# Kernel optimization log

Measured on AMD Instinct MI355X. Metric: run time of the kernel, lower is better.

## Reference

```python
import jax, jax.numpy as jnp
import numpy as np
import math

HEAD_DIM = 128
LAMBDA_INIT = 0.8
GN_EPS = 1e-05
NEG = -1e9


def ghostmax(scores):
    # softmax with an extra implicit zero logit (softmax-plus-one)
    m = jnp.maximum(jnp.max(scores, axis=-1, keepdims=True), 0.0)
    e = jnp.exp(scores - m)
    return e / (jnp.sum(e, axis=-1, keepdims=True) + jnp.exp(-m))


def setup_inputs() -> dict:
    key = jax.random.key(0)
    ks = jax.random.split(key, 8)
    B, H2, H, S, D = 2, 16, 8, 2048, HEAD_DIM
    return {
        "q": jax.random.normal(ks[0], (B, H2, S, D), dtype=jnp.float32),
        "k": jax.random.normal(ks[1], (B, H2, S, D), dtype=jnp.float32),
        "v": jax.random.normal(ks[2], (B, H, S, D), dtype=jnp.float32),
        "lambda_q1": 0.1 * jax.random.normal(ks[3], (D,), dtype=jnp.float32),
        "lambda_k1": 0.1 * jax.random.normal(ks[4], (D,), dtype=jnp.float32),
        "lambda_q2": 0.1 * jax.random.normal(ks[5], (D,), dtype=jnp.float32),
        "lambda_k2": 0.1 * jax.random.normal(ks[6], (D,), dtype=jnp.float32),
        "gn_weight": jnp.ones((H * D,), dtype=jnp.float32),
        "gn_bias": jnp.zeros((H * D,), dtype=jnp.float32),
    }


def reference(q, k, v, lambda_q1, lambda_k1, lambda_q2, lambda_k2, gn_weight, gn_bias):
    B, H2, S, D = q.shape
    H = H2 // 2
    scaling = 1.0 / math.sqrt(D)
    # [B, 2H, S, S] attention scores
    scores = jnp.einsum("bhsd,bhtd->bhst", q, k) * scaling
    causal_mask = jnp.triu(jnp.full((S, S), NEG, dtype=scores.dtype), k=1)
    scores = scores + causal_mask[None, None]
    w = ghostmax(scores)
    w = w.reshape(B, H, 2, S, S)
    lam = (
        jnp.exp(jnp.sum(lambda_q1 * lambda_k1))
        - jnp.exp(jnp.sum(lambda_q2 * lambda_k2))
        + LAMBDA_INIT
    )
    w = w[:, :, 0] - lam * w[:, :, 1]  # [B, H, S, S]
    out = jnp.einsum("bhst,bhtd->bhsd", w, v)  # [B, H, S, D]
    # torch .reshape(B, -1, S): raw row-major reinterpretation
    out = out.reshape(B, H * D, S)
    # GroupNorm: num_groups=H over channels H*D, normalized over (group channels, seq)
    g = out.reshape(B, H, D * S)
    mean = jnp.mean(g, axis=-1, keepdims=True)
    var = jnp.var(g, axis=-1, keepdims=True)
    g = (g - mean) * jax.lax.rsqrt(var + GN_EPS)
    out = g.reshape(B, H * D, S) * gn_weight[None, :, None] + gn_bias[None, :, None]
    return out * (1.0 - LAMBDA_INIT)
```

## Files before the change

### kernel.cpp

```cpp
#include <hip/hip_runtime.h>
#include <hip/hip_bf16.h>
#include <cstddef>
#include <cstdint>


typedef __bf16 bf16x8 __attribute__((ext_vector_type(8)));
typedef __bf16 bf16x4 __attribute__((ext_vector_type(4)));
typedef float f32x4 __attribute__((ext_vector_type(4)));

constexpr int SEQ = 2048;
constexpr int DH  = 128;
constexpr int NH  = 8;
constexpr int NH2 = 16;
constexpr float SCALE  = 0.088388347648318447f;
constexpr float QSCALE = 0.127517430f;

template <bool B> struct BoolK { static constexpr bool value = B; };

constexpr size_t QK_ELEMS = (size_t)2 * NH2 * SEQ * DH;
constexpr size_t V_ELEMS  = (size_t)2 * NH  * SEQ * DH;
constexpr size_t OFF_KB   = 4096;
constexpr size_t OFF_VT   = OFF_KB + QK_ELEMS * 2;
constexpr size_t WS_NEED  = OFF_VT + V_ELEMS * 2;

__device__ __forceinline__ void load_lds16(const void* g, void* l) {
  __builtin_amdgcn_global_load_lds(
      (const __attribute__((address_space(1))) uint32_t*)g,
      (__attribute__((address_space(3))) uint32_t*)l, 16, 0, 0);
}

__device__ __forceinline__ bf16x8 cvt8(float4 a, float4 b) {
  bf16x8 r;
  r[0] = (__bf16)a.x; r[1] = (__bf16)a.y; r[2] = (__bf16)a.z; r[3] = (__bf16)a.w;
  r[4] = (__bf16)b.x; r[5] = (__bf16)b.y; r[6] = (__bf16)b.z; r[7] = (__bf16)b.w;
  return r;
}

__global__ __launch_bounds__(256) void prep_kernel(
    const float* __restrict__ k, const float* __restrict__ v,
    __bf16* __restrict__ Kb, __bf16* __restrict__ Vtb,
    float* __restrict__ stats)
{
  __shared__ float tile[32][33];
  const int id = blockIdx.x;
  if (id == 0 && threadIdx.x < 64) stats[threadIdx.x] = 0.f;
  if (id < 4096) {
    const size_t i = ((size_t)id * 256 + threadIdx.x) * 8;
    float4 a = *(const float4*)(k + i);
    float4 b = *(const float4*)(k + i + 4);
    *(bf16x8*)(Kb + i) = cvt8(a, b);
  } else {
    const int vid = id - 4096;
    const int tt = vid & 63, dt = (vid >> 6) & 3, bh = vid >> 8;
    const int tr = threadIdx.x >> 3, tc = (threadIdx.x & 7) * 4;
    const float* src = v + ((size_t)bh * SEQ + tt * 32) * DH + dt * 32;
    float4 f = *(const float4*)(src + (size_t)tr * DH + tc);
    tile[tr][tc + 0] = f.x; tile[tr][tc + 1] = f.y;
    tile[tr][tc + 2] = f.z; tile[tr][tc + 3] = f.w;
    __syncthreads();
    __bf16* dst = Vtb + ((size_t)bh * DH + dt * 32 + tr) * SEQ + tt * 32 + tc;
    bf16x4 o;
    o[0] = (__bf16)tile[tc + 0][tr];
    o[1] = (__bf16)tile[tc + 1][tr];
    o[2] = (__bf16)tile[tc + 2][tr];
    o[3] = (__bf16)tile[tc + 3][tr];
    *(bf16x4*)dst = o;
  }
}

__global__ __launch_bounds__(256, 2) void attn3_kernel(
    const float* __restrict__ Qf, const __bf16* __restrict__ Kb,
    const __bf16* __restrict__ Vtb,
    const float* __restrict__ lq1, const float* __restrict__ lk1,
    const float* __restrict__ lq2, const float* __restrict__ lk2,
    float* __restrict__ Obuf, float* __restrict__ stats)
{
  __shared__ __align__(16) __bf16 ldsK[2][2][32][128];
  __shared__ __align__(16) __bf16 ldsVt[2][128][32];
  __shared__ __align__(16) __bf16 ldsP[4][32][36];
  __shared__ float ldsLa[64];

  const int bid = (int)blockIdx.x;
  int qt, bh;
  if (bid < 256) { qt = 31 - (bid >> 4); bh = bid & 15; }
  else           { qt = (bid - 256) >> 4; bh = bid & 15; }
  const int b = bh >> 3, h = bh & 7;
  const int tid = threadIdx.x;
  const int wv = tid >> 6;
  const int g  = wv >> 1;
  const int w2 = wv & 1;
  const int lane = tid & 63;
  const int l15 = lane & 15, quad = lane >> 4;

  float a1 = lq1[lane]*lk1[lane] + lq1[lane+64]*lk1[lane+64];
  float a2 = lq2[lane]*lk2[lane] + lq2[lane+64]*lk2[lane+64];
  #pragma unroll
  for (int off = 1; off < 64; off <<= 1) {
    a1 += __shfl_xor(a1, off);
    a2 += __shfl_xor(a2, off);
  }
  const float lam = __expf(a1) - __expf(a2) + 0.8f;

  const size_t headQK = (size_t)(b*NH2 + 2*h + g) * SEQ * DH;
  const float*  Qh  = Qf + headQK;
  const __bf16* Kh  = Kb + headQK;
  const __bf16* Vth = Vtb + (size_t)(b*NH + h) * DH * SEQ;

  size_t goffK[4];
  #pragma unroll
  for (int i = 0; i < 4; ++i) {
    const int c  = i*128 + w2*64 + lane;
    const int R  = c >> 4, cs = c & 15;
    goffK[i] = (size_t)R * DH + ((cs ^ (R & 15)) * 8);
  }
  size_t goffV[2];
  #pragma unroll
  for (int i = 0; i < 2; ++i) {
    const int c  = i*256 + tid;
    const int d  = c >> 2, cs = c & 3;
    goffV[i] = (size_t)d * SEQ + ((cs ^ (d & 3)) * 8);
  }

  __bf16* ldsKg = &ldsK[g][0][0][0];
  __bf16* ldsVb = &ldsVt[0][0][0];

  const int qb = qt * 64;
  const int nsteps = 2*qt + 2;
  const int rbase = qb + w2*32;

  bf16x8 qf[2][4];
  #pragma unroll
  for (int mi = 0; mi < 2; ++mi) {
    const float* src = Qh + (size_t)(rbase + mi*16 + l15)*DH + quad*8;
    #pragma unroll
    for (int kd = 0; kd < 4; ++kd) {
      float4 f0 = *(const float4*)(src + kd*32);
      float4 f1 = *(const float4*)(src + kd*32 + 4);
      f0.x *= QSCALE; f0.y *= QSCALE; f0.z *= QSCALE; f0.w *= QSCALE;
      f1.x *= QSCALE; f1.y *= QSCALE; f1.z *= QSCALE; f1.w *= QSCALE;
      qf[mi][kd] = cvt8(f0, f1);
    }
  }

  f32x4 oacc[2][8];
  float lsum[2][4];
  #pragma unroll
  for (int mi = 0; mi < 2; ++mi) {
    #pragma unroll
    for (int nt = 0; nt < 8; ++nt) oacc[mi][nt] = (f32x4){0.f,0.f,0.f,0.f};
    #pragma unroll
    for (int r = 0; r < 4; ++r) lsum[mi][r] = 0.f;
  }

  {
    #pragma unroll
    for (int i = 0; i < 4; ++i)
      load_lds16(Kh + goffK[i], ldsKg + i*1024 + w2*512);
    #pragma unroll
    for (int i = 0; i < 2; ++i)
      load_lds16(Vth + goffV[i], ldsVb + i*2048 + wv*512);
  }
  __syncthreads();

  for (int st = 0; st < nsteps; ++st) {
    const int cur = st & 1;
    const int kbt = st * 32;

    if (st + 1 < nsteps) {
      const int nxt = cur ^ 1;
      const __bf16* kg = Kh + (size_t)(kbt + 32) * DH;
      #pragma unroll
      for (int i = 0; i < 4; ++i)
        load_lds16(kg + goffK[i], ldsKg + nxt*4096 + i*1024 + w2*512);
      #pragma unroll
      for (int i = 0; i < 2; ++i)
        load_lds16(Vth + (kbt + 32) + goffV[i], ldsVb + nxt*4096 + i*2048 + wv*512);
    }

    f32x4 sacc[2][2];
    #pragma unroll
    for (int mi = 0; mi < 2; ++mi) {
      sacc[mi][0] = (f32x4){0.f,0.f,0.f,0.f};
      sacc[mi][1] = (f32x4){0.f,0.f,0.f,0.f};
    }
    __builtin_amdgcn_s_setprio(1);
    #pragma unroll
    for (int n = 0; n < 2; ++n)
      #pragma unroll
      for (int kd = 0; kd < 4; ++kd) {
        bf16x8 kf = *(const bf16x8*)&ldsK[g][cur][n*16 + l15][((kd*4 + quad) ^ l15) * 8];
        sacc[0][n] = __builtin_amdgcn_mfma_f32_16x16x32_bf16(qf[0][kd], kf, sacc[0][n], 0, 0, 0);
        sacc[1][n] = __builtin_amdgcn_mfma_f32_16x16x32_bf16(qf[1][kd], kf, sacc[1][n], 0, 0, 0);
      }
    __builtin_amdgcn_s_setprio(0);

    auto sm_body = [&](auto MASKC) {
      constexpr bool MASKED = decltype(MASKC)::value;
      #pragma unroll
      for (int mi = 0; mi < 2; ++mi)
        #pragma unroll
        for (int r = 0; r < 4; ++r) {
          float p0 = __builtin_amdgcn_exp2f(sacc[mi][0][r]);
          float p1 = __builtin_amdgcn_exp2f(sacc[mi][1][r]);
          if constexpr (MASKED) {
            const int qr = rbase + mi*16 + quad*4 + r;
            if (kbt + l15      > qr) p0 = 0.f;
            if (kbt + l15 + 16 > qr) p1 = 0.f;
          }
          lsum[mi][r] += p0 + p1;
          ldsP[wv][mi*16 + quad*4 + r][l15]      = (__bf16)p0;
          ldsP[wv][mi*16 + quad*4 + r][l15 + 16] = (__bf16)p1;
        }
    };
    if (kbt + 31 <= rbase) sm_body(BoolK<false>{});
    else                   sm_body(BoolK<true>{});

    {
      bf16x8 pf0 = *(const bf16x8*)&ldsP[wv][l15][quad*8];
      bf16x8 pf1 = *(const bf16x8*)&ldsP[wv][16 + l15][quad*8];
      __builtin_amdgcn_s_setprio(1);
      #pragma unroll
      for (int nt = 0; nt < 8; ++nt) {
        bf16x8 vf = *(const bf16x8*)&ldsVt[cur][nt*16 + l15][(quad ^ (l15 & 3)) * 8];
        oacc[0][nt] = __builtin_amdgcn_mfma_f32_16x16x32_bf16(pf0, vf, oacc[0][nt], 0, 0, 0);
        oacc[1][nt] = __builtin_amdgcn_mfma_f32_16x16x32_bf16(pf1, vf, oacc[1][nt], 0, 0, 0);
      }
      __builtin_amdgcn_s_setprio(0);
    }
    __syncthreads();
  }

  float lr[2][4];
  #pragma unroll
  for (int mi = 0; mi < 2; ++mi)
    #pragma unroll
    for (int r = 0; r < 4; ++r) {
      float vsum = lsum[mi][r];
      #pragma unroll
      for (int off = 1; off < 16; off <<= 1) vsum += __shfl_xor(vsum, off);
      lr[mi][r] = vsum;
    }

  float* Oscr = (float*)&ldsK[0][0][0][0];
  if (g == 1) {
    #pragma unroll
    for (int mi = 0; mi < 2; ++mi) {
      #pragma unroll
      for (int nt = 0; nt < 8; ++nt)
        #pragma unroll
        for (int r = 0; r < 4; ++r)
          Oscr[(w2*32 + mi*16 + quad*4 + r)*128 + nt*16 + l15] = oacc[mi][nt][r];
      if (l15 == 0) {
        #pragma unroll
        for (int r = 0; r < 4; ++r)
          ldsLa[w2*32 + mi*16 + quad*4 + r] = lr[mi][r];
      }
    }
  }
  __syncthreads();

  if (g == 0) {
    float* obase = Obuf + (size_t)(b*NH + h) * SEQ * DH;
    float sum = 0.f, ss = 0.f;
    #pragma unroll
    for (int mi = 0; mi < 2; ++mi)
      #pragma unroll
      for (int r = 0; r < 4; ++r) {
        const int row = w2*32 + mi*16 + quad*4 + r;
        const float l0 = lr[mi][r] + 1.0f;
        const float l1 = ldsLa[row] + 1.0f;
        const float i0 = 1.0f / l0;
        const float i1 = lam / l1;
        float* orow = obase + (size_t)(qb + row) * DH + l15;
        #pragma unroll
        for (int nt = 0; nt < 8; ++nt) {
          const float o1 = Oscr[row*128 + nt*16 + l15];
          const float val = oacc[mi][nt][r] * i0 - o1 * i1;
          orow[nt*16] = val;
          sum += val;
          ss  += val * val;
        }
      }
    #pragma unroll
    for (int off = 1; off < 64; off <<= 1) {
      sum += __shfl_xor(sum, off);
      ss  += __shfl_xor(ss, off);
    }
    if (lane == 0) {
      atomicAdd(&stats[2*(b*NH + h)],     sum);
      atomicAdd(&stats[2*(b*NH + h) + 1], ss);
    }
  }
}

__global__ __launch_bounds__(256) void attn_fb_kernel(
    const float* __restrict__ q, const float* __restrict__ k,
    const float* __restrict__ v,
    const float* __restrict__ lq1, const float* __restrict__ lk1,
    const float* __restrict__ lq2, const float* __restrict__ lk2,
    float* __restrict__ Obuf, float* __restrict__ stats)
{
  __shared__ __align__(16) __bf16 lds_k[2][32][136];
  __shared__ __align__(16) __bf16 lds_vt[128][40];
  __shared__ __align__(16) __bf16 lds_p[4][2][16][40];

  const int qt = blockIdx.x, h = blockIdx.y, b = blockIdx.z;
  const int qb = qt * 64;
  const int tid = threadIdx.x;
  const int w = tid >> 6, lane = tid & 63;
  const int l15 = lane & 15, quad = lane >> 4;

  float a1 = lq1[lane]*lk1[lane] + lq1[lane+64]*lk1[lane+64];
  float a2 = lq2[lane]*lk2[lane] + lq2[lane+64]*lk2[lane+64];
  #pragma unroll
  for (int off = 1; off < 64; off <<= 1) {
    a1 += __shfl_xor(a1, off);
    a2 += __shfl_xor(a2, off);
  }
  const float lam = __expf(a1) - __expf(a2) + 0.8f;

  const float* qh0 = q + (size_t)(b*NH2 + 2*h) * SEQ * DH;
  const float* qh1 = qh0 + (size_t)SEQ * DH;
  const float* kh0 = k + (size_t)(b*NH2 + 2*h) * SEQ * DH;
  const float* kh1 = kh0 + (size_t)SEQ * DH;
  const float* vh  = v + (size_t)(b*NH + h) * SEQ * DH;

  bf16x8 qf[2][4];
  {
    const int qrow = qb + w*16 + l15;
    #pragma unroll
    for (int sh = 0; sh < 2; ++sh) {
      const float* src = (sh ? qh1 : qh0) + (size_t)qrow * DH + quad*8;
      #pragma unroll
      for (int kd = 0; kd < 4; ++kd) {
        float4 f0 = *(const float4*)(src + kd*32);
        float4 f1 = *(const float4*)(src + kd*32 + 4);
        qf[sh][kd] = cvt8(f0, f1);
      }
    }
  }

  f32x4 oacc[2][8];
  #pragma unroll
  for (int sh = 0; sh < 2; ++sh)
    #pragma unroll
    for (int nt = 0; nt < 8; ++nt)
      oacc[sh][nt] = (f32x4){0.f,0.f,0.f,0.f};

  float mst[2][4] = {{0.f,0.f,0.f,0.f},{0.f,0.f,0.f,0.f}};
  float lst[2][4] = {{1.f,1.f,1.f,1.f},{1.f,1.f,1.f,1.f}};

  const int krow = tid >> 2, ksh = krow >> 5, kr = krow & 31;
  const int kd0 = (tid & 3) * 32;
  const float* ksrc0 = (ksh ? kh1 : kh0) + kd0;
  const int vt = tid >> 3, vd = (tid & 7) * 16;

  const int nsteps = (qb + 64) / 32;
  for (int st = 0; st < nsteps; ++st) {
    const int kbt = st * 32;
    {
      const float* sp = ksrc0 + (size_t)(kbt + kr) * DH;
      #pragma unroll
      for (int c = 0; c < 4; ++c) {
        float4 f0 = *(const float4*)(sp + c*8);
        float4 f1 = *(const float4*)(sp + c*8 + 4);
        *(bf16x8*)&lds_k[ksh][kr][kd0 + c*8] = cvt8(f0, f1);
      }
      const float* vp = vh + (size_t)(kbt + vt) * DH + vd;
      #pragma unroll
      for (int c = 0; c < 4; ++c) {
        float4 f = *(const float4*)(vp + c*4);
        lds_vt[vd + c*4 + 0][vt] = (__bf16)f.x;
        lds_vt[vd + c*4 + 1][vt] = (__bf16)f.y;
        lds_vt[vd + c*4 + 2][vt] = (__bf16)f.z;
        lds_vt[vd + c*4 + 3][vt] = (__bf16)f.w;
      }
    }
    __syncthreads();

    f32x4 sacc[2][2];
    #pragma unroll
    for (int sh = 0; sh < 2; ++sh)
      #pragma unroll
      for (int n = 0; n < 2; ++n)
        sacc[sh][n] = (f32x4){0.f,0.f,0.f,0.f};

    #pragma unroll
    for (int sh = 0; sh < 2; ++sh)
      #pragma unroll
      for (int n = 0; n < 2; ++n)
        #pragma unroll
        for (int kd = 0; kd < 4; ++kd) {
          bf16x8 bf = *(const bf16x8*)&lds_k[sh][n*16 + l15][kd*32 + quad*8];
          sacc[sh][n] = __builtin_amdgcn_mfma_f32_16x16x32_bf16(qf[sh][kd], bf, sacc[sh][n], 0, 0, 0);
        }

    const int qrow0 = qb + w*16 + quad*4;
    const int c0 = kbt + l15, c1 = c0 + 16;
    #pragma unroll
    for (int sh = 0; sh < 2; ++sh) {
      #pragma unroll
      for (int r = 0; r < 4; ++r) {
        float s0 = sacc[sh][0][r] * SCALE;
        float s1 = sacc[sh][1][r] * SCALE;
        const int qr = qrow0 + r;
        if (c0 > qr) s0 = -1e30f;
        if (c1 > qr) s1 = -1e30f;
        float mx = fmaxf(s0, s1);
        #pragma unroll
        for (int off = 1; off < 16; off <<= 1)
          mx = fmaxf(mx, __shfl_xor(mx, off));
        const float mnew = fmaxf(mst[sh][r], mx);
        const float alpha = __expf(mst[sh][r] - mnew);
        mst[sh][r] = mnew;
        const float p0 = __expf(s0 - mnew);
        const float p1 = __expf(s1 - mnew);
        float rs = p0 + p1;
        #pragma unroll
        for (int off = 1; off < 16; off <<= 1)
          rs += __shfl_xor(rs, off);
        lst[sh][r] = lst[sh][r] * alpha + rs;
        #pragma unroll
        for (int nt = 0; nt < 8; ++nt)
          oacc[sh][nt][r] *= alpha;
        lds_p[w][sh][quad*4 + r][l15]      = (__bf16)p0;
        lds_p[w][sh][quad*4 + r][l15 + 16] = (__bf16)p1;
      }
    }

    {
      bf16x8 pf0 = *(const bf16x8*)&lds_p[w][0][l15][quad*8];
      bf16x8 pf1 = *(const bf16x8*)&lds_p[w][1][l15][quad*8];
      #pragma unroll
      for (int nt = 0; nt < 8; ++nt) {
        bf16x8 vf = *(const bf16x8*)&lds_vt[nt*16 + l15][quad*8];
        oacc[0][nt] = __builtin_amdgcn_mfma_f32_16x16x32_bf16(pf0, vf, oacc[0][nt], 0, 0, 0);
        oacc[1][nt] = __builtin_amdgcn_mfma_f32_16x16x32_bf16(pf1, vf, oacc[1][nt], 0, 0, 0);
      }
    }
    __syncthreads();
  }

  const int qrow0 = qb + w*16 + quad*4;
  float* obase = Obuf + (size_t)(b*NH + h) * SEQ * DH;
  float sum = 0.f, ss = 0.f;
  #pragma unroll
  for (int r = 0; r < 4; ++r) {
    const float i0 = 1.0f / lst[0][r];
    const float i1 = lam / lst[1][r];
    float* orow = obase + (size_t)(qrow0 + r) * DH + l15;
    #pragma unroll
    for (int nt = 0; nt < 8; ++nt) {
      const float val = oacc[0][nt][r] * i0 - oacc[1][nt][r] * i1;
      orow[nt*16] = val;
      sum += val;
      ss  += val * val;
    }
  }
  #pragma unroll
  for (int off = 1; off < 64; off <<= 1) {
    sum += __shfl_xor(sum, off);
    ss  += __shfl_xor(ss, off);
  }
  if (lane == 0) {
    atomicAdd(&stats[2*(b*NH + h)],     sum);
    atomicAdd(&stats[2*(b*NH + h) + 1], ss);
  }
}

__global__ __launch_bounds__(256) void norm_kernel(
    float* __restrict__ Obuf, const float* __restrict__ stats,
    const float* __restrict__ gw, const float* __restrict__ gb)
{
  const int idx = (blockIdx.x * 256 + threadIdx.x) * 4;
  const int bh = idx >> 18;
  const int local = idx & 262143;
  const float inv = 1.0f / 262144.0f;
  const float mean = stats[2*bh] * inv;
  const float var  = stats[2*bh + 1] * inv - mean * mean;
  const float rstd = rsqrtf(var + 1e-5f);
  const int c = ((bh & 7) << 7) + (local >> 11);
  const float wq = gw[c] * rstd;
  const float bq = gb[c];
  float4 o = *(const float4*)(Obuf + idx);
  float4 r;
  r.x = ((o.x - mean) * wq + bq) * 0.2f;
  r.y = ((o.y - mean) * wq + bq) * 0.2f;
  r.z = ((o.z - mean) * wq + bq) * 0.2f;
  r.w = ((o.w - mean) * wq + bq) * 0.2f;
  *(float4*)(Obuf + idx) = r;
}

extern "C" void kernel_launch(void* const* d_in, const int* in_sizes, int n_in,
                              void* d_out, int out_size, void* d_ws, size_t ws_size,
                              hipStream_t stream) {
  const float* q   = (const float*)d_in[0];
  const float* k   = (const float*)d_in[1];
  const float* v   = (const float*)d_in[2];
  const float* lq1 = (const float*)d_in[3];
  const float* lk1 = (const float*)d_in[4];
  const float* lq2 = (const float*)d_in[5];
  const float* lk2 = (const float*)d_in[6];
  const float* gw  = (const float*)d_in[7];
  const float* gb  = (const float*)d_in[8];
  float* out = (float*)d_out;
  float* stats = (float*)d_ws;

  if (ws_size >= WS_NEED) {
    __bf16* Kb  = (__bf16*)((char*)d_ws + OFF_KB);
    __bf16* Vtb = (__bf16*)((char*)d_ws + OFF_VT);

    prep_kernel<<<8192, 256, 0, stream>>>(k, v, Kb, Vtb, stats);

    attn3_kernel<<<512, 256, 0, stream>>>(q, Kb, Vtb,
        lq1, lk1, lq2, lk2, out, stats);
  } else {
    (void)hipMemsetAsync(d_ws, 0, 256, stream);
    attn_fb_kernel<<<dim3(32, NH, 2), 256, 0, stream>>>(q, k, v,
        lq1, lk1, lq2, lk2, out, stats);
  }

  const int total = 2 * NH * SEQ * DH;
  norm_kernel<<<total / 1024, 256, 0, stream>>>(out, stats, gw, gb);
}
```

Baseline: 212.7 us.

## Pair light and heavy query tiles per block and keep P in registers

Each block now handles two 32-row query tiles, a light one (pair) and a heavy one (63-pair), so every block walks the same total number of causal key steps, replacing the earlier 64-row tile with a split ordering. The score MFMA operands are swapped to produce transposed S, so the probabilities can be packed to bf16 and rearranged with cross-lane shuffles into the PV operand instead of going through an LDS staging buffer. This is meant to balance work across blocks and remove LDS writes and reads for P. The cost is extra shuffles and selects, plus a branch per step on whether the light tile is still active.

```diff
diff --git a/kernel.cpp b/kernel.cpp
--- a/kernel.cpp
+++ b/kernel.cpp
@@ -34,6 +34,12 @@
   r[0] = (__bf16)a.x; r[1] = (__bf16)a.y; r[2] = (__bf16)a.z; r[3] = (__bf16)a.w;
   r[4] = (__bf16)b.x; r[5] = (__bf16)b.y; r[6] = (__bf16)b.z; r[7] = (__bf16)b.w;
   return r;
+}
+
+__device__ __forceinline__ uint32_t pk2(float lo, float hi) {
+  union { __bf16 h[2]; uint32_t u; } t;
+  t.h[0] = (__bf16)lo; t.h[1] = (__bf16)hi;
+  return t.u;
 }
 
 __global__ __launch_bounds__(256) void prep_kernel(
@@ -77,13 +83,12 @@
 {
   __shared__ __align__(16) __bf16 ldsK[2][2][32][128];
   __shared__ __align__(16) __bf16 ldsVt[2][128][32];
-  __shared__ __align__(16) __bf16 ldsP[4][32][36];
   __shared__ float ldsLa[64];
 
   const int bid = (int)blockIdx.x;
-  int qt, bh;
-  if (bid < 256) { qt = 31 - (bid >> 4); bh = bid & 15; }
-  else           { qt = (bid - 256) >> 4; bh = bid & 15; }
+  const int pair = bid >> 4;
+  const int bh = bid & 15;
+  const int qtA = pair, qtB = 63 - pair;
   const int b = bh >> 3, h = bh & 7;
   const int tid = threadIdx.x;
   const int wv = tid >> 6;
@@ -124,33 +129,66 @@
   __bf16* ldsKg = &ldsK[g][0][0][0];
   __bf16* ldsVb = &ldsVt[0][0][0];
 
-  const int qb = qt * 64;
-  const int nsteps = 2*qt + 2;
-  const int rbase = qb + w2*32;
-
-  bf16x8 qf[2][4];
+  const int nsteps = qtB + 1;
+  const int qrowA = qtA*32 + w2*16 + l15;
+  const int qrowB = qtB*32 + w2*16 + l15;
+
+  bf16x8 qfA[4], qfB[4];
   #pragma unroll
   for (int mi = 0; mi < 2; ++mi) {
-    const float* src = Qh + (size_t)(rbase + mi*16 + l15)*DH + quad*8;
+    const float* src = Qh + (size_t)(mi ? qrowB : qrowA)*DH + quad*8;
     #pragma unroll
     for (int kd = 0; kd < 4; ++kd) {
       float4 f0 = *(const float4*)(src + kd*32);
       float4 f1 = *(const float4*)(src + kd*32 + 4);
       f0.x *= QSCALE; f0.y *= QSCALE; f0.z *= QSCALE; f0.w *= QSCALE;
       f1.x *= QSCALE; f1.y *= QSCALE; f1.z *= QSCALE; f1.w *= QSCALE;
-      qf[mi][kd] = cvt8(f0, f1);
-    }
-  }
-
-  f32x4 oacc[2][8];
-  float lsum[2][4];
-  #pragma unroll
-  for (int mi = 0; mi < 2; ++mi) {
-    #pragma unroll
-    for (int nt = 0; nt < 8; ++nt) oacc[mi][nt] = (f32x4){0.f,0.f,0.f,0.f};
-    #pragma unroll
-    for (int r = 0; r < 4; ++r) lsum[mi][r] = 0.f;
-  }
+      (mi ? qfB : qfA)[kd] = cvt8(f0, f1);
+    }
+  }
+
+  f32x4 oaccA[8], oaccB[8];
+  float lsum[2] = {0.f, 0.f};
+  #pragma unroll
+  for (int nt = 0; nt < 8; ++nt) {
+    oaccA[nt] = (f32x4){0.f,0.f,0.f,0.f};
+    oaccB[nt] = (f32x4){0.f,0.f,0.f,0.f};
+  }
+
+  auto smx = [&](const f32x4 s0, const f32x4 s1, const int qrow,
+                 const int kbt, float& ls, auto MASKC) -> bf16x8 {
+    constexpr bool MASKED = decltype(MASKC)::value;
+    float p0[4], p1[4];
+    #pragma unroll
+    for (int r = 0; r < 4; ++r) {
+      p0[r] = __builtin_amdgcn_exp2f(s0[r]);
+      p1[r] = __builtin_amdgcn_exp2f(s1[r]);
+      if constexpr (MASKED) {
+        if (kbt + quad*4 + r      > qrow) p0[r] = 0.f;
+        if (kbt + 16 + quad*4 + r > qrow) p1[r] = 0.f;
+      }
+    }
+    ls += ((p0[0] + p0[1]) + (p0[2] + p0[3]))
+        + ((p1[0] + p1[1]) + (p1[2] + p1[3]));
+    const uint32_t a0 = pk2(p0[0], p0[1]), b0 = pk2(p0[2], p0[3]);
+    const uint32_t a1 = pk2(p1[0], p1[1]), b1 = pk2(p1[2], p1[3]);
+    const uint32_t s16a = (quad & 2) ? a1 : a0;
+    const uint32_t s16b = (quad & 2) ? b1 : b0;
+    const uint32_t s32a = (quad & 2) ? a0 : a1;
+    const uint32_t s32b = (quad & 2) ? b0 : b1;
+    const uint32_t r16a = __shfl_xor((int)s16a, 16);
+    const uint32_t r16b = __shfl_xor((int)s16b, 16);
+    const uint32_t r32a = __shfl_xor((int)s32a, 32);
+    const uint32_t r32b = __shfl_xor((int)s32b, 32);
+    const uint32_t r48a = __shfl_xor((int)r32a, 16);
+    const uint32_t r48b = __shfl_xor((int)r32b, 16);
+    union { uint32_t u[4]; bf16x8 v; } o;
+    o.u[0] = (quad == 0) ? a0   : (quad == 1) ? r48a : (quad == 2) ? r32a : r16a;
+    o.u[1] = (quad == 0) ? b0   : (quad == 1) ? r48b : (quad == 2) ? r32b : r16b;
+    o.u[2] = (quad == 0) ? r16a : (quad == 1) ? r32a : (quad == 2) ? r48a : a1;
+    o.u[3] = (quad == 0) ? r16b : (quad == 1) ? r32b : (quad == 2) ? r48b : b1;
+    return o.v;
+  };
 
   {
     #pragma unroll
@@ -165,6 +203,7 @@
   for (int st = 0; st < nsteps; ++st) {
     const int cur = st & 1;
     const int kbt = st * 32;
+    const bool aact = (st <= qtA);
 
     if (st + 1 < nsteps) {
       const int nxt = cur ^ 1;
@@ -177,84 +216,83 @@
         load_lds16(Vth + (kbt + 32) + goffV[i], ldsVb + nxt*4096 + i*2048 + wv*512);
     }
 
-    f32x4 sacc[2][2];
-    #pragma unroll
-    for (int mi = 0; mi < 2; ++mi) {
-      sacc[mi][0] = (f32x4){0.f,0.f,0.f,0.f};
-      sacc[mi][1] = (f32x4){0.f,0.f,0.f,0.f};
-    }
+    f32x4 sA[2], sB[2];
+    sA[0] = (f32x4){0.f,0.f,0.f,0.f}; sA[1] = (f32x4){0.f,0.f,0.f,0.f};
+    sB[0] = (f32x4){0.f,0.f,0.f,0.f}; sB[1] = (f32x4){0.f,0.f,0.f,0.f};
     __builtin_amdgcn_s_setprio(1);
-    #pragma unroll
-    for (int n = 0; n < 2; ++n)
-      #pragma unroll
-      for (int kd = 0; kd < 4; ++kd) {
-        bf16x8 kf = *(const bf16x8*)&ldsK[g][cur][n*16 + l15][((kd*4 + quad) ^ l15) * 8];
-        sacc[0][n] = __builtin_amdgcn_mfma_f32_16x16x32_bf16(qf[0][kd], kf, sacc[0][n], 0, 0, 0);
-        sacc[1][n] = __builtin_amdgcn_mfma_f32_16x16x32_bf16(qf[1][kd], kf, sacc[1][n], 0, 0, 0);
-      }
+    if (aact) {
+      #pragma unroll
+      for (int n = 0; n < 2; ++n)
+        #pragma unroll
+        for (int kd = 0; kd < 4; ++kd) {
+          bf16x8 kf = *(const bf16x8*)&ldsK[g][cur][n*16 + l15][((kd*4 + quad) ^ l15) * 8];
+          sB[n] = __builtin_amdgcn_mfma_f32_16x16x32_bf16(kf, qfB[kd], sB[n], 0, 0, 0);
+          sA[n] = __builtin_amdgcn_mfma_f32_16x16x32_bf16(kf, qfA[kd], sA[n], 0, 0, 0);
+        }
+    } else {
+      #pragma unroll
+      for (int n = 0; n < 2; ++n)
+        #pragma unroll
+        for (int kd = 0; kd < 4; ++kd) {
+          bf16x8 kf = *(const bf16x8*)&ldsK[g][cur][n*16 + l15][((kd*4 + quad) ^ l15) * 8];
+          sB[n] = __builtin_amdgcn_mfma_f32_16x16x32_bf16(kf, qfB[kd], sB[n], 0, 0, 0);
+        }
+    }
     __builtin_amdgcn_s_setprio(0);
 
-    auto sm_body = [&](auto MASKC) {
-      constexpr bool MASKED = decltype(MASKC)::value;
-      #pragma unroll
-      for (int mi = 0; mi < 2; ++mi)
-        #pragma unroll
-        for (int r = 0; r < 4; ++r) {
-          float p0 = __builtin_amdgcn_exp2f(sacc[mi][0][r]);
-          float p1 = __builtin_amdgcn_exp2f(sacc[mi][1][r]);
-          if constexpr (MASKED) {
-            const int qr = rbase + mi*16 + quad*4 + r;
-            if (kbt + l15      > qr) p0 = 0.f;
-            if (kbt + l15 + 16 > qr) p1 = 0.f;
-          }
-          lsum[mi][r] += p0 + p1;
-          ldsP[wv][mi*16 + quad*4 + r][l15]      = (__bf16)p0;
-          ldsP[wv][mi*16 + quad*4 + r][l15 + 16] = (__bf16)p1;
-        }
-    };
-    if (kbt + 31 <= rbase) sm_body(BoolK<false>{});
-    else                   sm_body(BoolK<true>{});
-
-    {
-      bf16x8 pf0 = *(const bf16x8*)&ldsP[wv][l15][quad*8];
-      bf16x8 pf1 = *(const bf16x8*)&ldsP[wv][16 + l15][quad*8];
-      __builtin_amdgcn_s_setprio(1);
+    bf16x8 pfA, pfB;
+    if (st < qtA) {
+      pfA = smx(sA[0], sA[1], qrowA, kbt, lsum[0], BoolK<false>{});
+      pfB = smx(sB[0], sB[1], qrowB, kbt, lsum[1], BoolK<false>{});
+    } else if (st == qtA) {
+      pfA = smx(sA[0], sA[1], qrowA, kbt, lsum[0], BoolK<true>{});
+      pfB = smx(sB[0], sB[1], qrowB, kbt, lsum[1], BoolK<false>{});
+    } else if (st == qtB) {
+      pfB = smx(sB[0], sB[1], qrowB, kbt, lsum[1], BoolK<true>{});
+    } else {
+      pfB = smx(sB[0], sB[1], qrowB, kbt, lsum[1], BoolK<false>{});
+    }
+
+    __builtin_amdgcn_s_setprio(1);
+    if (aact) {
       #pragma unroll
       for (int nt = 0; nt < 8; ++nt) {
         bf16x8 vf = *(const bf16x8*)&ldsVt[cur][nt*16 + l15][(quad ^ (l15 & 3)) * 8];
-        oacc[0][nt] = __builtin_amdgcn_mfma_f32_16x16x32_bf16(pf0, vf, oacc[0][nt], 0, 0, 0);
-        oacc[1][nt] = __builtin_amdgcn_mfma_f32_16x16x32_bf16(pf1, vf, oacc[1][nt], 0, 0, 0);
-      }
-      __builtin_amdgcn_s_setprio(0);
-    }
+        oaccB[nt] = __builtin_amdgcn_mfma_f32_16x16x32_bf16(pfB, vf, oaccB[nt], 0, 0, 0);
+        oaccA[nt] = __builtin_amdgcn_mfma_f32_16x16x32_bf16(pfA, vf, oaccA[nt], 0, 0, 0);
+      }
+    } else {
+      #pragma unroll
+      for (int nt = 0; nt < 8; ++nt) {
+        bf16x8 vf = *(const bf16x8*)&ldsVt[cur][nt*16 + l15][(quad ^ (l15 & 3)) * 8];
+        oaccB[nt] = __builtin_amdgcn_mfma_f32_16x16x32_bf16(pfB, vf, oaccB[nt], 0, 0, 0);
+      }
+    }
+    __builtin_amdgcn_s_setprio(0);
     __syncthreads();
   }
 
-  float lr[2][4];
-  #pragma unroll
-  for (int mi = 0; mi < 2; ++mi)
-    #pragma unroll
-    for (int r = 0; r < 4; ++r) {
-      float vsum = lsum[mi][r];
-      #pragma unroll
-      for (int off = 1; off < 16; off <<= 1) vsum += __shfl_xor(vsum, off);
-      lr[mi][r] = vsum;
-    }
+  float lr[2];
+  #pragma unroll
+  for (int mi = 0; mi < 2; ++mi) {
+    float v = lsum[mi];
+    v += __shfl_xor(v, 16);
+    v += __shfl_xor(v, 32);
+    lr[mi] = v;
+  }
 
   float* Oscr = (float*)&ldsK[0][0][0][0];
   if (g == 1) {
     #pragma unroll
     for (int mi = 0; mi < 2; ++mi) {
+      f32x4* oa = mi ? oaccB : oaccA;
       #pragma unroll
       for (int nt = 0; nt < 8; ++nt)
         #pragma unroll
         for (int r = 0; r < 4; ++r)
-          Oscr[(w2*32 + mi*16 + quad*4 + r)*128 + nt*16 + l15] = oacc[mi][nt][r];
-      if (l15 == 0) {
-        #pragma unroll
-        for (int r = 0; r < 4; ++r)
-          ldsLa[w2*32 + mi*16 + quad*4 + r] = lr[mi][r];
-      }
+          Oscr[(mi*32 + w2*16 + quad*4 + r)*128 + nt*16 + l15] = oa[nt][r];
+      if (lane < 16)
+        ldsLa[mi*32 + w2*16 + lane] = lr[mi];
     }
   }
   __syncthreads();
@@ -263,24 +301,27 @@
     float* obase = Obuf + (size_t)(b*NH + h) * SEQ * DH;
     float sum = 0.f, ss = 0.f;
     #pragma unroll
-    for (int mi = 0; mi < 2; ++mi)
+    for (int mi = 0; mi < 2; ++mi) {
+      f32x4* oa = mi ? oaccB : oaccA;
+      const int qb = (mi ? qtB : qtA) * 32;
       #pragma unroll
       for (int r = 0; r < 4; ++r) {
-        const int row = w2*32 + mi*16 + quad*4 + r;
-        const float l0 = lr[mi][r] + 1.0f;
-        const float l1 = ldsLa[row] + 1.0f;
+        const int row16 = quad*4 + r;
+        const float l0 = __shfl(lr[mi], row16) + 1.0f;
+        const float l1 = ldsLa[mi*32 + w2*16 + row16] + 1.0f;
         const float i0 = 1.0f / l0;
         const float i1 = lam / l1;
-        float* orow = obase + (size_t)(qb + row) * DH + l15;
+        float* orow = obase + (size_t)(qb + w2*16 + row16) * DH + l15;
         #pragma unroll
         for (int nt = 0; nt < 8; ++nt) {
-          const float o1 = Oscr[row*128 + nt*16 + l15];
-          const float val = oacc[mi][nt][r] * i0 - o1 * i1;
+          const float o1 = Oscr[(mi*32 + w2*16 + row16)*128 + nt*16 + l15];
+          const float val = oa[nt][r] * i0 - o1 * i1;
           orow[nt*16] = val;
           sum += val;
           ss  += val * val;
         }
       }
+    }
     #pragma unroll
     for (int off = 1; off < 64; off <<= 1) {
       sum += __shfl_xor(sum, off);
```

After: 220.8 us. 1.04x slower.
